# Kernel tuning notes

Hardware: AMD Instinct MI355X
Metric: run time of the kernel (lower is better)

Reference implementation:

```python
import jax, jax.numpy as jnp
import numpy as np

NUM_ITERATIONS = 3  # matches init kwarg num_iterations
B, R, CIN, COUT, K = 32, 2048, 64, 64, 16


def squash(s):
    # squash along the last (capsule-vector) axis, as in the torch module
    sq = jnp.sum(s * s, axis=-1, keepdims=True)
    return (sq / (1.0 + sq)) * s / jnp.sqrt(sq)


def setup_inputs() -> dict:
    key = jax.random.key(0)
    k1, k2 = jax.random.split(key)
    x = jax.random.normal(k1, (B, R, CIN), dtype=jnp.float32)
    route_weights = jax.random.normal(k2, (K, R, CIN, COUT), dtype=jnp.float32) * 0.05
    return {"x": x, "route_weights": route_weights}


def reference(x, route_weights):
    # priors[k,b,r,o] = sum_c x[b,r,c] * W[k,r,c,o]   -> [K, B, R, COUT]
    priors = jnp.einsum('brc,krco->kbro', x, route_weights)
    logits = jnp.zeros(priors.shape[:3] + (1,), dtype=priors.dtype)  # [K,B,R,1]
    outputs = None
    for i in range(NUM_ITERATIONS):
        probs = jax.nn.softmax(logits, axis=2)  # softmax over route nodes (torch dim=2)
        outputs = squash(jnp.sum(probs * priors, axis=2, keepdims=True))  # [K,B,1,COUT]
        if i != NUM_ITERATIONS - 1:
            logits = logits + jnp.sum(priors * outputs, axis=-1, keepdims=True)
    return outputs[:, :, 0, :]  # [K, B, COUT]
```

## Files before the change

### kernel.cpp

```cpp
#include <hip/hip_runtime.h>
#include <hip/hip_bf16.h>
#include <stdint.h>

#define NB 32
#define NR 2048
#define NC 64
#define NO 64
#define NK 16

using bf16x8 = __attribute__((ext_vector_type(8))) short;
using f32x4  = __attribute__((ext_vector_type(4))) float;

#define WAITVM(N) do { asm volatile("s_waitcnt vmcnt(" #N ")" ::: "memory"); \
                       __builtin_amdgcn_sched_barrier(0); } while (0)

__device__ __forceinline__ uint32_t f2bf(float f) {
  uint32_t u = __builtin_bit_cast(uint32_t, f);
  return (u + 0x7fffu + ((u >> 16) & 1u)) >> 16;
}
__device__ __forceinline__ uint32_t packbf2(float lo, float hi) {
  return f2bf(lo) | (f2bf(hi) << 16);
}
__device__ __forceinline__ uint32_t cvtpk2(float lo, float hi) {
  float2 v; v.x = lo; v.y = hi;
  __hip_bfloat162 h = __float22bfloat162_rn(v);
  uint32_t r;
  __builtin_memcpy(&r, &h, 4);
  return r;
}

__device__ __forceinline__ void gload_lds16(const float* g, float* l) {
  __builtin_amdgcn_global_load_lds(
      (const __attribute__((address_space(1))) void*)g,
      (__attribute__((address_space(3))) void*)l, 16, 0, 0);
}

__global__ __launch_bounds__(256) void make_xbf(const float* __restrict__ x,
                                                ushort* __restrict__ xbf) {
  __shared__ float tile[32][72];
  const int r = blockIdx.x, t = threadIdx.x;
  {
    const int b = t >> 3, c0 = (t & 7) << 3;
    const float* xp = x + ((size_t)b * NR + r) * NC + c0;
    *(float4*)&tile[b][c0] = *(const float4*)xp;
    *(float4*)&tile[b][c0 + 4] = *(const float4*)(xp + 4);
  }
  __syncthreads();
  {
    const int ks = t >> 7, mt = (t >> 6) & 1, l = t & 63;
    const int b = mt * 16 + (l & 15);
    const int cb = ks * 32 + (l >> 4) * 8;
    uint4 uv;
    uv.x = packbf2(tile[b][cb + 0], tile[b][cb + 1]);
    uv.y = packbf2(tile[b][cb + 2], tile[b][cb + 3]);
    uv.z = packbf2(tile[b][cb + 4], tile[b][cb + 5]);
    uv.w = packbf2(tile[b][cb + 6], tile[b][cb + 7]);
    *(uint4*)(xbf + (size_t)r * 2048 + t * 8) = uv;
  }
}

__global__ __launch_bounds__(256, 2) void priors_gemm(const ushort* __restrict__ xbf,
                                                      const float* __restrict__ W,
                                                      ushort* __restrict__ priors) {
  __shared__ float ldsW[2][4][2048];
  __shared__ ushort ldsE[4][2048];
  const int w = threadIdx.x >> 6, lane = threadIdx.x & 63;
  const int g = lane >> 4, col = lane & 15;
  const int kq = blockIdx.x & 3, rblk = blockIdx.x >> 2;
  const int k = kq * 4 + w;

  f32x4 acc[2][4];

  auto stage = [&](int rr, int ks, int buf) {
    const float* srcrow = W + ((size_t)(k * NR + rblk * 8 + rr)) * 4096 + ks * 2048;
    float* dst = &ldsW[buf][w][0] + lane * 4;
    const int j = lane & 15;
#pragma unroll
    for (int i = 0; i < 8; ++i) {
      const int c = i * 4 + (lane >> 4);
      const int gc = c >> 3;
      const int jj = j ^ (gc & 3) ^ ((gc >> 1) << 2);
      gload_lds16(srcrow + c * 64 + jj * 4, dst + i * 256);
    }
  };

  auto compute = [&](bf16x8 af0, bf16x8 af1, int buf) {
    const float* pw = &ldsW[buf][w][0];
#pragma unroll
    for (int nt = 0; nt < 4; ++nt) {
      const int oo = (nt * 16 + col) ^ ((g & 3) << 2) ^ ((g >> 1) << 4);
      float f[8];
#pragma unroll
      for (int e = 0; e < 8; ++e) f[e] = pw[(g * 8 + e) * 64 + oo];
      uint4 uv;
      uv.x = cvtpk2(f[0], f[1]);
      uv.y = cvtpk2(f[2], f[3]);
      uv.z = cvtpk2(f[4], f[5]);
      uv.w = cvtpk2(f[6], f[7]);
      bf16x8 bfr = __builtin_bit_cast(bf16x8, uv);
      acc[0][nt] = __builtin_amdgcn_mfma_f32_16x16x32_bf16(af0, bfr, acc[0][nt], 0, 0, 0);
      acc[1][nt] = __builtin_amdgcn_mfma_f32_16x16x32_bf16(af1, bfr, acc[1][nt], 0, 0, 0);
    }
  };

  auto epilogue = [&](int rr) {
    ushort* ep = &ldsE[w][0];
#pragma unroll
    for (int mt = 0; mt < 2; ++mt)
#pragma unroll
      for (int nt = 0; nt < 4; ++nt)
#pragma unroll
        for (int rp = 0; rp < 2; ++rp) {
          uint32_t u = cvtpk2(acc[mt][nt][rp * 2], acc[mt][nt][rp * 2 + 1]);
          const int row0 = mt * 16 + g * 4 + rp * 2;
          ep[(row0 + 0) * 64 + nt * 16 + col] = (ushort)u;
          ep[(row0 + 1) * 64 + nt * 16 + col] = (ushort)(u >> 16);
        }
    ushort* pp = priors + ((size_t)(k * NR + rblk * 8 + rr)) * 2048;
#pragma unroll
    for (int i = 0; i < 4; ++i) {
      uint4 v = *(const uint4*)(ep + lane * 8 + i * 512);
      *(uint4*)(pp + lane * 8 + i * 512) = v;
    }
  };

  stage(0, 0, 0);
  for (int ti = 0; ti < 8; ++ti) {
    const size_t r = rblk * 8 + ti;
    bf16x8 a00 = *(const bf16x8*)(xbf + ((r * 2 + 0) * 2 + 0) * 512 + lane * 8);
    bf16x8 a10 = *(const bf16x8*)(xbf + ((r * 2 + 0) * 2 + 1) * 512 + lane * 8);
    bf16x8 a01 = *(const bf16x8*)(xbf + ((r * 2 + 1) * 2 + 0) * 512 + lane * 8);
    bf16x8 a11 = *(const bf16x8*)(xbf + ((r * 2 + 1) * 2 + 1) * 512 + lane * 8);
    stage(ti, 1, 1);
#pragma unroll
    for (int mt = 0; mt < 2; ++mt)
#pragma unroll
      for (int nt = 0; nt < 4; ++nt) acc[mt][nt] = f32x4{0.f, 0.f, 0.f, 0.f};
    WAITVM(12);
    compute(a00, a10, 0);
    if (ti < 7) {
      stage(ti + 1, 0, 0);
      WAITVM(8);
    } else {
      WAITVM(0);
    }
    compute(a01, a11, 1);
    epilogue(ti);
  }
}

template <int PASS>
__global__ __launch_bounds__(256) void routing(const __hip_bfloat16* __restrict__ priors,
                                               float* __restrict__ Abuf,
                                               const float* __restrict__ o_prev,
                                               float* __restrict__ o_out) {
  __shared__ float o_lds[64];
  __shared__ float red_num[4][8][8];
  __shared__ float red_den[4];
  const int kb = blockIdx.x;
  const int k = kb >> 5, b = kb & 31;
  const int tid = threadIdx.x, w = tid >> 6, lane = tid & 63;
  const int g = lane >> 3, sl = lane & 7;
  const int rsub = w * 8 + g;
  const __hip_bfloat16* pbase = priors + (size_t)k * NR * NB * NO + (size_t)b * NO;
  float* ab = Abuf + (size_t)kb * NR;

  if (PASS == 1) {
    float sum[8];
#pragma unroll
    for (int j = 0; j < 8; ++j) sum[j] = 0.f;
    for (int it = 0; it < NR / 32; ++it) {
      const int r = it * 32 + rsub;
      uint4 pv = *(const uint4*)(pbase + (size_t)r * (NB * NO) + sl * 8);
      sum[0] += __builtin_bit_cast(float, pv.x << 16);
      sum[1] += __builtin_bit_cast(float, pv.x & 0xffff0000u);
      sum[2] += __builtin_bit_cast(float, pv.y << 16);
      sum[3] += __builtin_bit_cast(float, pv.y & 0xffff0000u);
      sum[4] += __builtin_bit_cast(float, pv.z << 16);
      sum[5] += __builtin_bit_cast(float, pv.z & 0xffff0000u);
      sum[6] += __builtin_bit_cast(float, pv.w << 16);
      sum[7] += __builtin_bit_cast(float, pv.w & 0xffff0000u);
    }
#pragma unroll
    for (int m = 8; m < 64; m <<= 1)
#pragma unroll
      for (int j = 0; j < 8; ++j) sum[j] += __shfl_xor(sum[j], m, 64);
    if (lane < 8) {
#pragma unroll
      for (int j = 0; j < 8; ++j) red_num[w][lane][j] = sum[j];
    }
    __syncthreads();
    if (tid < 64) {
      const int s_ = tid >> 3, j_ = tid & 7;
      float sv = (red_num[0][s_][j_] + red_num[1][s_][j_] +
                  red_num[2][s_][j_] + red_num[3][s_][j_]) * (1.f / (float)NR);
      float sq = sv * sv;
#pragma unroll
      for (int m = 1; m < 64; m <<= 1) sq += __shfl_xor(sq, m, 64);
      o_lds[tid] = (sq / (1.f + sq)) * rsqrtf(sq) * sv;
    }
    __syncthreads();
  } else {
    if (tid < 64) o_lds[tid] = o_prev[kb * 64 + tid];
    __syncthreads();
  }

  float os[8];
#pragma unroll
  for (int j = 0; j < 8; ++j) os[j] = o_lds[sl * 8 + j];

  float num[8];
#pragma unroll
  for (int j = 0; j < 8; ++j) num[j] = 0.f;
  float den = 0.f;

  for (int it = 0; it < NR / 32; ++it) {
    const int r = it * 32 + rsub;
    uint4 pv = *(const uint4*)(pbase + (size_t)r * (NB * NO) + sl * 8);
    float f[8];
    f[0] = __builtin_bit_cast(float, pv.x << 16);
    f[1] = __builtin_bit_cast(float, pv.x & 0xffff0000u);
    f[2] = __builtin_bit_cast(float, pv.y << 16);
    f[3] = __builtin_bit_cast(float, pv.y & 0xffff0000u);
    f[4] = __builtin_bit_cast(float, pv.z << 16);
    f[5] = __builtin_bit_cast(float, pv.z & 0xffff0000u);
    f[6] = __builtin_bit_cast(float, pv.w << 16);
    f[7] = __builtin_bit_cast(float, pv.w & 0xffff0000u);

    float d = 0.f;
#pragma unroll
    for (int j = 0; j < 8; ++j) d = fmaf(f[j], os[j], d);
#pragma unroll
    for (int m = 1; m < 8; m <<= 1) d += __shfl_xor(d, m, 64);

    float lg;
    if (PASS == 1) {
      lg = d;
      if (sl == 0) ab[r] = d;
    } else {
      lg = d + ab[r];
    }
    float e = __expf(lg);
    den += e;
#pragma unroll
    for (int j = 0; j < 8; ++j) num[j] = fmaf(e, f[j], num[j]);
  }

#pragma unroll
  for (int m = 8; m < 64; m <<= 1) {
    den += __shfl_xor(den, m, 64);
#pragma unroll
    for (int j = 0; j < 8; ++j) num[j] += __shfl_xor(num[j], m, 64);
  }
  if (lane < 8) {
#pragma unroll
    for (int j = 0; j < 8; ++j) red_num[w][lane][j] = num[j];
    if (lane == 0) red_den[w] = den;
  }
  __syncthreads();

  if (tid < 64) {
    const int s_ = tid >> 3, j_ = tid & 7;
    float nm = red_num[0][s_][j_] + red_num[1][s_][j_] + red_num[2][s_][j_] + red_num[3][s_][j_];
    float dn = red_den[0] + red_den[1] + red_den[2] + red_den[3];
    float sv = nm / dn;
    float sq = sv * sv;
#pragma unroll
    for (int m = 1; m < 64; m <<= 1) sq += __shfl_xor(sq, m, 64);
    float ov = (sq / (1.f + sq)) * rsqrtf(sq) * sv;
    o_out[kb * 64 + tid] = ov;
  }
}

extern "C" void kernel_launch(void* const* d_in, const int* in_sizes, int n_in,
                              void* d_out, int out_size, void* d_ws, size_t ws_size,
                              hipStream_t stream) {
  const float* x = (const float*)d_in[0];
  const float* W = (const float*)d_in[1];
  float* out = (float*)d_out;
  char* ws = (char*)d_ws;

  size_t off = 0;
  ushort* xbf = (ushort*)(ws + off);               off += (size_t)NR * 2048 * 2;
  ushort* priors = (ushort*)(ws + off);            off += (size_t)NK * NR * NB * NO * 2;
  float* o1 = (float*)(ws + off);                  off += (size_t)NK * NB * NO * 4;
  float* Abuf = (float*)(ws + off);                off += (size_t)NK * NB * NR * 4;

  make_xbf<<<NR, 256, 0, stream>>>(x, xbf);
  priors_gemm<<<(NR / 8) * (NK / 4), 256, 0, stream>>>(xbf, W, priors);
  routing<1><<<NK * NB, 256, 0, stream>>>((const __hip_bfloat16*)priors, Abuf, nullptr, o1);
  routing<2><<<NK * NB, 256, 0, stream>>>((const __hip_bfloat16*)priors, Abuf, o1, out);
}
```

Before: 238.4 us.

## Stage W tiles through registers instead of direct global-to-LDS loads

Replaces the global_load_lds direct-to-LDS staging of W with a register double-buffer (two banks of 8 float4 per lane) followed by explicit ds_writes into the per-wave LDS buffers. Loads for the next half-tile are issued before each compute phase, and the vmcnt waits are placed so the LDS write follows that compute. The aim is to overlap W fetch latency with MFMA work more flexibly and to avoid the constraints of the direct-LDS load path. In exchange it uses 64 extra VGPRs under a 2-block occupancy bound and adds extra LDS write instructions.

```diff
diff --git a/kernel.cpp b/kernel.cpp
--- a/kernel.cpp
+++ b/kernel.cpp
@@ -27,12 +27,6 @@
   uint32_t r;
   __builtin_memcpy(&r, &h, 4);
   return r;
-}
-
-__device__ __forceinline__ void gload_lds16(const float* g, float* l) {
-  __builtin_amdgcn_global_load_lds(
-      (const __attribute__((address_space(1))) void*)g,
-      (__attribute__((address_space(3))) void*)l, 16, 0, 0);
 }
 
 __global__ __launch_bounds__(256) void make_xbf(const float* __restrict__ x,
@@ -68,21 +62,33 @@
   const int g = lane >> 4, col = lane & 15;
   const int kq = blockIdx.x & 3, rblk = blockIdx.x >> 2;
   const int k = kq * 4 + w;
+  const float* wbase = W + ((size_t)(k * NR + rblk * 8)) * 4096;
 
   f32x4 acc[2][4];
-
-  auto stage = [&](int rr, int ks, int buf) {
-    const float* srcrow = W + ((size_t)(k * NR + rblk * 8 + rr)) * 4096 + ks * 2048;
-    float* dst = &ldsW[buf][w][0] + lane * 4;
-    const int j = lane & 15;
-#pragma unroll
-    for (int i = 0; i < 8; ++i) {
-      const int c = i * 4 + (lane >> 4);
-      const int gc = c >> 3;
-      const int jj = j ^ (gc & 3) ^ ((gc >> 1) << 2);
-      gload_lds16(srcrow + c * 64 + jj * 4, dst + i * 256);
-    }
-  };
+  float4 RA[8], RB[8];
+
+  int srcoff[8];
+#pragma unroll
+  for (int i = 0; i < 8; ++i) {
+    const int c = i * 4 + (lane >> 4);
+    const int gc = c >> 3;
+    const int jj = (lane & 15) ^ (gc & 3) ^ ((gc >> 1) << 2);
+    srcoff[i] = c * 64 + jj * 4;
+  }
+
+#define LOADW(BANK, H)                                                        \
+  do {                                                                        \
+    const float* src_ = wbase + (size_t)(H) * 2048;                           \
+    _Pragma("unroll") for (int i_ = 0; i_ < 8; ++i_)                          \
+      BANK[i_] = *(const float4*)(src_ + srcoff[i_]);                         \
+  } while (0)
+
+#define DSWRITE(BANK, BUF)                                                    \
+  do {                                                                        \
+    float* dst_ = &ldsW[BUF][w][0] + lane * 4;                                \
+    _Pragma("unroll") for (int i_ = 0; i_ < 8; ++i_)                          \
+      *(float4*)(dst_ + i_ * 256) = BANK[i_];                                 \
+  } while (0)
 
   auto compute = [&](bf16x8 af0, bf16x8 af1, int buf) {
     const float* pw = &ldsW[buf][w][0];
@@ -124,27 +130,34 @@
     }
   };
 
-  stage(0, 0, 0);
+  LOADW(RA, 0);
+  WAITVM(0);
+  DSWRITE(RA, 0);
+  LOADW(RB, 1);
+
   for (int ti = 0; ti < 8; ++ti) {
     const size_t r = rblk * 8 + ti;
+    const int h0 = ti * 2;
     bf16x8 a00 = *(const bf16x8*)(xbf + ((r * 2 + 0) * 2 + 0) * 512 + lane * 8);
     bf16x8 a10 = *(const bf16x8*)(xbf + ((r * 2 + 0) * 2 + 1) * 512 + lane * 8);
     bf16x8 a01 = *(const bf16x8*)(xbf + ((r * 2 + 1) * 2 + 0) * 512 + lane * 8);
     bf16x8 a11 = *(const bf16x8*)(xbf + ((r * 2 + 1) * 2 + 1) * 512 + lane * 8);
-    stage(ti, 1, 1);
 #pragma unroll
     for (int mt = 0; mt < 2; ++mt)
 #pragma unroll
       for (int nt = 0; nt < 4; ++nt) acc[mt][nt] = f32x4{0.f, 0.f, 0.f, 0.f};
-    WAITVM(12);
+
+    if (h0 + 2 < 16) LOADW(RA, h0 + 2);
     compute(a00, a10, 0);
-    if (ti < 7) {
-      stage(ti + 1, 0, 0);
+    WAITVM(8);
+    DSWRITE(RB, 1);
+
+    if (h0 + 3 < 16) LOADW(RB, h0 + 3);
+    compute(a01, a11, 1);
+    if (h0 + 2 < 16) {
       WAITVM(8);
-    } else {
-      WAITVM(0);
-    }
-    compute(a01, a11, 1);
+      DSWRITE(RA, 0);
+    }
     epilogue(ti);
   }
 }
```

Result: slower. 285.1 us (+19.6%).
